# Optimization experiments

Measured on AMD Instinct MI355X. Metric: run time of the kernel, lower is better.

Reference implementation:

```python
import jax, jax.numpy as jnp
import numpy as np

TABLE_NUM = 16
TABLE_SIZE_LOG2 = 12
T = 1 << TABLE_SIZE_LOG2          # 4096 entries per table
FEAT = 2                          # features per entry (mini_linear in = table_num*2)
Z_DIM = 512
RES_MIN = 16
RES_MAX = 256
IMG = 256
MLP_HIDDEN = 64
OUT_DIM = 3
BATCH = 8
PRIME_Y = np.uint32(2654435761)   # instant-NGP spatial hash prime


def setup_inputs() -> dict:
    key = jax.random.key(0)
    ks = jax.random.split(key, 9)
    d_tab = TABLE_NUM * T * FEAT
    return {
        "z": jax.random.normal(ks[0], (BATCH, Z_DIM), jnp.float32),
        "w_table": jax.random.normal(ks[1], (Z_DIM, d_tab), jnp.float32) * 1e-2,
        "b_table": jnp.zeros((d_tab,), jnp.float32),
        "w1": jax.random.normal(ks[2], (TABLE_NUM * FEAT, MLP_HIDDEN), jnp.float32) * (1.0 / np.sqrt(TABLE_NUM * FEAT)),
        "b1": jnp.zeros((MLP_HIDDEN,), jnp.float32),
        "w2": jax.random.normal(ks[3], (MLP_HIDDEN, MLP_HIDDEN), jnp.float32) * (1.0 / np.sqrt(MLP_HIDDEN)),
        "b2": jnp.zeros((MLP_HIDDEN,), jnp.float32),
        "w3": jax.random.normal(ks[4], (MLP_HIDDEN, OUT_DIM), jnp.float32) * (1.0 / np.sqrt(MLP_HIDDEN)),
        "b3": jnp.zeros((OUT_DIM,), jnp.float32),
    }


def _sample_coords(b):
    c = (jnp.arange(IMG, dtype=jnp.float32) + 0.5) / IMG
    xx, yy = jnp.meshgrid(c, c, indexing="ij")  # torch.meshgrid default
    coords = jnp.stack([xx, yy], axis=-1).reshape(1, -1, 2)
    return jnp.broadcast_to(coords, (b, IMG * IMG, 2))


def _hash_retrieve(tables, coords):
    """tables: B x L x T x F; coords: B x N x 2 in [0,1). Returns B x N x (L*F)."""
    B, L, _, _ = tables.shape
    growth = np.exp((np.log(RES_MAX) - np.log(RES_MIN)) / (L - 1))
    offs = jnp.array([[0, 0], [1, 0], [0, 1], [1, 1]], dtype=jnp.uint32)  # 4 corners
    bidx = jnp.arange(B)[:, None, None]
    feats = []
    for l in range(L):
        res = jnp.float32(RES_MIN * (growth ** l))
        pos = coords * res                      # B,N,2
        pos0 = jnp.floor(pos)
        frac = pos - pos0                       # B,N,2
        corner = pos0.astype(jnp.uint32)[:, :, None, :] + offs[None, None]  # B,N,4,2
        idx = (corner[..., 0] ^ (corner[..., 1] * PRIME_Y)) & jnp.uint32(T - 1)
        f = tables[:, l][bidx, idx.astype(jnp.int32)]        # B,N,4,F gather
        fx, fy = frac[..., 0], frac[..., 1]
        w = jnp.stack([(1 - fx) * (1 - fy), fx * (1 - fy),
                       (1 - fx) * fy,       fx * fy], axis=-1)  # B,N,4
        feats.append(jnp.einsum("bncf,bnc->bnf", f, w))
    return jnp.concatenate(feats, axis=-1)


def reference(z, w_table, b_table, w1, b1, w2, b2, w3, b3):
    B = z.shape[0]
    tables = (z @ w_table + b_table).reshape(B, TABLE_NUM, T, FEAT)
    coords = _sample_coords(B).astype(tables.dtype)
    feat = _hash_retrieve(tables, coords)                    # B,N,L*F
    h = jax.nn.relu(feat @ w1 + b1)
    h = jax.nn.relu(h @ w2 + b2)
    o = jnp.tanh(h @ w3 + b3)                                # B,N,3
    return o.reshape(B, IMG, IMG, OUT_DIM).transpose(0, 3, 1, 2)
```

## Files before the change

### kernel.cpp

```cpp
#include <hip/hip_runtime.h>
#include <cmath>

#define TABLE_NUM 16
#define T_SIZE    4096
#define Z_DIM     512
#define IMG       256
#define D_TAB     (TABLE_NUM * T_SIZE * 2)
#define BATCH     8
#define HID       64
#define N_PIX     (IMG * IMG)
#define PRIME_Y   2654435761u
#define KCHUNK    4
#define KLEN      (Z_DIM / KCHUNK)
#define NG4       (D_TAB / 4)

typedef _Float16 v8h  __attribute__((ext_vector_type(8)));
typedef _Float16 v2h  __attribute__((ext_vector_type(2)));
typedef float    v4f  __attribute__((ext_vector_type(4)));

struct ResArr { float r[TABLE_NUM]; };

__global__ void prep_weights(const float* __restrict__ w1, const float* __restrict__ w2,
                             const float* __restrict__ w3, const float* __restrict__ z,
                             _Float16* __restrict__ w1T, _Float16* __restrict__ w2T,
                             _Float16* __restrict__ w3T, float* __restrict__ zT)
{
    const int t = threadIdx.x;
    for (int i = t; i < HID * 32; i += 256) {
        int n = i >> 5, k = i & 31;
        w1T[i] = (_Float16)w1[k * HID + n];
    }
    for (int i = t; i < HID * HID; i += 256) {
        int n = i >> 6, k = i & 63;
        w2T[i] = (_Float16)w2[k * HID + n];
    }
    for (int i = t; i < 16 * HID; i += 256) {
        int n = i >> 6, k = i & 63;
        w3T[i] = (_Float16)(n < 3 ? w3[k * 3 + n] : 0.f);
    }
    for (int i = t; i < Z_DIM * BATCH; i += 256) {
        int k = i >> 3, b = i & 7;
        zT[i] = z[b * Z_DIM + k];
    }
}

__global__ __launch_bounds__(256) void gen_partial(
    const float* __restrict__ zT, const float* __restrict__ w,
    float* __restrict__ part)
{
    const int c  = blockIdx.x >> 7;
    const int g  = (blockIdx.x & 127) * 256 + threadIdx.x;
    const int k0 = c * KLEN;
    const float4* wp = reinterpret_cast<const float4*>(w) + g;

    float4 acc[BATCH];
#pragma unroll
    for (int b = 0; b < BATCH; ++b) acc[b] = make_float4(0.f, 0.f, 0.f, 0.f);

#pragma unroll 8
    for (int kk = 0; kk < KLEN; ++kk) {
        const int k = k0 + kk;
        float4 wv = wp[(size_t)k * NG4];
        const float* zr = zT + k * BATCH;
#pragma unroll
        for (int b = 0; b < BATCH; ++b) {
            float zv = zr[b];
            acc[b].x = fmaf(zv, wv.x, acc[b].x);
            acc[b].y = fmaf(zv, wv.y, acc[b].y);
            acc[b].z = fmaf(zv, wv.z, acc[b].z);
            acc[b].w = fmaf(zv, wv.w, acc[b].w);
        }
    }

    float4* pp = reinterpret_cast<float4*>(part);
#pragma unroll
    for (int b = 0; b < BATCH; ++b)
        pp[((size_t)(c * BATCH + b) << 15) + g] = acc[b];
}

__global__ __launch_bounds__(256) void gen_reduce(
    const float* __restrict__ part, const float* __restrict__ bt,
    float* __restrict__ tabs)
{
    const int i = blockIdx.x * 256 + threadIdx.x;
    const int b = i >> 15, g = i & (NG4 - 1);
    const float4* pp = reinterpret_cast<const float4*>(part);

    float4 s = pp[((size_t)(0 * BATCH + b) << 15) + g];
#pragma unroll
    for (int c = 1; c < KCHUNK; ++c) {
        float4 p = pp[((size_t)(c * BATCH + b) << 15) + g];
        s.x += p.x; s.y += p.y; s.z += p.z; s.w += p.w;
    }
    float4 bv = reinterpret_cast<const float4*>(bt)[g];
    s.x += bv.x; s.y += bv.y; s.z += bv.z; s.w += bv.w;
    reinterpret_cast<float4*>(tabs)[((size_t)b << 15) + g] = s;
}

__global__ __launch_bounds__(256) void hash_mlp(
    const float* __restrict__ tabs,
    const _Float16* __restrict__ w1T, const _Float16* __restrict__ w2T,
    const _Float16* __restrict__ w3T,
    const float* __restrict__ b1, const float* __restrict__ b2,
    const float* __restrict__ b3,
    float* __restrict__ out, ResArr res)
{
    __shared__ _Float16 mbuf[4][64][72];
    const int tid  = threadIdx.x;
    const int wid  = tid >> 6;
    const int lane = tid & 63;
    const int b    = blockIdx.x & 7;
    const int tile = blockIdx.x >> 3;
    const int ti   = tile >> 4;
    const int tj   = tile & 15;
    const int i0   = ti * 16 + wid * 4;
    const int j0   = tj * 16;

    const int di = lane >> 4, dj = lane & 15;
    const float cx = ((float)(i0 + di) + 0.5f) * (1.0f / IMG);
    const float cy = ((float)(j0 + dj) + 0.5f) * (1.0f / IMG);
    const float* tb = tabs + (size_t)b * D_TAB;
    const float2* tb2 = reinterpret_cast<const float2*>(tb);

#pragma unroll 4
    for (int l = 0; l < TABLE_NUM; ++l) {
        float r  = res.r[l];
        float px = cx * r, py = cy * r;
        float fx0 = floorf(px), fy0 = floorf(py);
        float fx = px - fx0, fy = py - fy0;
        unsigned x0 = (unsigned)(int)fx0, y0 = (unsigned)(int)fy0;
        unsigned hy0 = y0 * PRIME_Y, hy1 = (y0 + 1u) * PRIME_Y;
        unsigned i00 = (x0 ^ hy0) & (T_SIZE - 1);
        unsigned i10 = ((x0 + 1u) ^ hy0) & (T_SIZE - 1);
        unsigned i01 = (x0 ^ hy1) & (T_SIZE - 1);
        unsigned i11 = ((x0 + 1u) ^ hy1) & (T_SIZE - 1);
        const float2* tl = tb2 + l * T_SIZE;
        float2 f00 = tl[i00], f10 = tl[i10], f01 = tl[i01], f11 = tl[i11];
        float w00 = (1.f - fx) * (1.f - fy);
        float w10 = fx * (1.f - fy);
        float w01 = (1.f - fx) * fy;
        float w11 = fx * fy;
        float e0 = f00.x * w00 + f10.x * w10 + f01.x * w01 + f11.x * w11;
        float e1 = f00.y * w00 + f10.y * w10 + f01.y * w01 + f11.y * w11;
        v2h p; p.x = (_Float16)e0; p.y = (_Float16)e1;
        *reinterpret_cast<v2h*>(&mbuf[wid][lane][2 * l]) = p;
    }

    const int arow = lane & 15;
    const int kgrp = lane >> 4;

    float bias1v[4], bias2v[4];
#pragma unroll
    for (int nt = 0; nt < 4; ++nt) {
        bias1v[nt] = b1[nt * 16 + arow];
        bias2v[nt] = b2[nt * 16 + arow];
    }
    const float bias3 = (arow < 3) ? b3[arow] : 0.f;

    v8h bf1[4], bf2a[4], bf2b[4];
#pragma unroll
    for (int nt = 0; nt < 4; ++nt) {
        bf1[nt]  = *reinterpret_cast<const v8h*>(&w1T[(nt * 16 + arow) * 32 + kgrp * 8]);
        bf2a[nt] = *reinterpret_cast<const v8h*>(&w2T[(nt * 16 + arow) * 64 + kgrp * 8]);
        bf2b[nt] = *reinterpret_cast<const v8h*>(&w2T[(nt * 16 + arow) * 64 + 32 + kgrp * 8]);
    }
    v8h bf3a = *reinterpret_cast<const v8h*>(&w3T[arow * 64 + kgrp * 8]);
    v8h bf3b = *reinterpret_cast<const v8h*>(&w3T[arow * 64 + 32 + kgrp * 8]);

    v8h a1[4];
#pragma unroll
    for (int mt = 0; mt < 4; ++mt)
        a1[mt] = *reinterpret_cast<const v8h*>(&mbuf[wid][mt * 16 + arow][kgrp * 8]);

    v4f c1[4][4];
#pragma unroll
    for (int nt = 0; nt < 4; ++nt)
#pragma unroll
        for (int mt = 0; mt < 4; ++mt) {
            v4f c = {0.f, 0.f, 0.f, 0.f};
            c = __builtin_amdgcn_mfma_f32_16x16x32_f16(a1[mt], bf1[nt], c, 0, 0, 0);
#pragma unroll
            for (int e = 0; e < 4; ++e)
                c1[mt][nt][e] = fmaxf(c[e] + bias1v[nt], 0.f);
        }

#pragma unroll
    for (int mt = 0; mt < 4; ++mt)
#pragma unroll
        for (int nt = 0; nt < 4; ++nt)
#pragma unroll
            for (int e = 0; e < 4; ++e)
                mbuf[wid][mt * 16 + kgrp * 4 + e][nt * 16 + arow] = (_Float16)c1[mt][nt][e];

    v8h a2[4][2];
#pragma unroll
    for (int mt = 0; mt < 4; ++mt) {
        a2[mt][0] = *reinterpret_cast<const v8h*>(&mbuf[wid][mt * 16 + arow][kgrp * 8]);
        a2[mt][1] = *reinterpret_cast<const v8h*>(&mbuf[wid][mt * 16 + arow][32 + kgrp * 8]);
    }
    v4f c2[4][4];
#pragma unroll
    for (int nt = 0; nt < 4; ++nt)
#pragma unroll
        for (int mt = 0; mt < 4; ++mt) {
            v4f c = {0.f, 0.f, 0.f, 0.f};
            c = __builtin_amdgcn_mfma_f32_16x16x32_f16(a2[mt][0], bf2a[nt], c, 0, 0, 0);
            c = __builtin_amdgcn_mfma_f32_16x16x32_f16(a2[mt][1], bf2b[nt], c, 0, 0, 0);
#pragma unroll
            for (int e = 0; e < 4; ++e)
                c2[mt][nt][e] = fmaxf(c[e] + bias2v[nt], 0.f);
        }

#pragma unroll
    for (int mt = 0; mt < 4; ++mt)
#pragma unroll
        for (int nt = 0; nt < 4; ++nt)
#pragma unroll
            for (int e = 0; e < 4; ++e)
                mbuf[wid][mt * 16 + kgrp * 4 + e][nt * 16 + arow] = (_Float16)c2[mt][nt][e];

#pragma unroll
    for (int mt = 0; mt < 4; ++mt) {
        v8h a0  = *reinterpret_cast<const v8h*>(&mbuf[wid][mt * 16 + arow][kgrp * 8]);
        v8h a1v = *reinterpret_cast<const v8h*>(&mbuf[wid][mt * 16 + arow][32 + kgrp * 8]);
        v4f c = {0.f, 0.f, 0.f, 0.f};
        c = __builtin_amdgcn_mfma_f32_16x16x32_f16(a0,  bf3a, c, 0, 0, 0);
        c = __builtin_amdgcn_mfma_f32_16x16x32_f16(a1v, bf3b, c, 0, 0, 0);
        if (arow < 3) {
            float4 st;
            st.x = tanhf(c[0] + bias3);
            st.y = tanhf(c[1] + bias3);
            st.z = tanhf(c[2] + bias3);
            st.w = tanhf(c[3] + bias3);
            size_t idx = ((size_t)b * 3 + arow) * N_PIX
                       + (size_t)(i0 + mt) * IMG + j0 + kgrp * 4;
            *reinterpret_cast<float4*>(&out[idx]) = st;
        }
    }
}

extern "C" void kernel_launch(void* const* d_in, const int* in_sizes, int n_in,
                              void* d_out, int out_size, void* d_ws, size_t ws_size,
                              hipStream_t stream)
{
    const float* z  = (const float*)d_in[0];
    const float* wt = (const float*)d_in[1];
    const float* bt = (const float*)d_in[2];
    const float* w1 = (const float*)d_in[3];
    const float* b1 = (const float*)d_in[4];
    const float* w2 = (const float*)d_in[5];
    const float* b2 = (const float*)d_in[6];
    const float* w3 = (const float*)d_in[7];
    const float* b3 = (const float*)d_in[8];
    float* out  = (float*)d_out;

    char* ws = (char*)d_ws;
    float*     tabs = (float*)ws;
    float*     part = (float*)(ws + (4 << 20));
    _Float16*  w1T  = (_Float16*)(ws + (20 << 20));
    _Float16*  w2T  = (_Float16*)(ws + (20 << 20) + 4096);
    _Float16*  w3T  = (_Float16*)(ws + (20 << 20) + 12288);
    float*     zT   = (float*)(ws + (20 << 20) + 16384);

    ResArr ra;
    const double growth = std::exp((std::log(256.0) - std::log(16.0)) / 15.0);
    for (int l = 0; l < TABLE_NUM; ++l)
        ra.r[l] = (float)(16.0 * std::pow(growth, (double)l));

    prep_weights<<<1, 256, 0, stream>>>(w1, w2, w3, z, w1T, w2T, w3T, zT);
    gen_partial<<<KCHUNK * (NG4 / 256), 256, 0, stream>>>(zT, wt, part);
    gen_reduce<<<BATCH * NG4 / 256, 256, 0, stream>>>(part, bt, tabs);
    hash_mlp<<<BATCH * (N_PIX / 256), 256, 0, stream>>>(
        tabs, w1T, w2T, w3T, b1, b2, b3, out, ra);
}
```

Before: 99.37 us.

## Stage per-tile hash-grid cells in LDS before bilinear interpolation

For each 16x16 pixel tile, the block first gathers every hash-table entry its pixels can touch at each of the 16 levels into a shared-memory buffer, sized by a per-level cell capacity. Each pixel then reads its four corners from LDS instead of issuing four scattered global gathers per level. This aims to cut redundant global and L2 gather traffic, since neighbouring pixels share corners. In exchange it adds about 10 KB of LDS per block, a block-wide barrier and a staging phase, and it relies on the hard-coded capacities covering every tile footprint.

```diff
diff --git a/kernel.cpp b/kernel.cpp
--- a/kernel.cpp
+++ b/kernel.cpp
@@ -20,6 +20,10 @@
 
 struct ResArr { float r[TABLE_NUM]; };
 
+__device__ constexpr int WCAP[16]  = {3,4,4,4,5,5,5,6,7,8,9,10,11,13,15,18};
+__device__ constexpr int CBASE[16] = {0,9,25,41,57,82,107,132,168,217,281,362,462,583,752,977};
+#define CTOT 1301
+
 __global__ void prep_weights(const float* __restrict__ w1, const float* __restrict__ w2,
                              const float* __restrict__ w3, const float* __restrict__ z,
                              _Float16* __restrict__ w1T, _Float16* __restrict__ w2T,
@@ -86,7 +90,7 @@
     const int b = i >> 15, g = i & (NG4 - 1);
     const float4* pp = reinterpret_cast<const float4*>(part);
 
-    float4 s = pp[((size_t)(0 * BATCH + b) << 15) + g];
+    float4 s = pp[((size_t)b << 15) + g];
 #pragma unroll
     for (int c = 1; c < KCHUNK; ++c) {
         float4 p = pp[((size_t)(c * BATCH + b) << 15) + g];
@@ -106,36 +110,56 @@
     float* __restrict__ out, ResArr res)
 {
     __shared__ _Float16 mbuf[4][64][72];
+    __shared__ float2   cstage[CTOT];
+
     const int tid  = threadIdx.x;
     const int wid  = tid >> 6;
     const int lane = tid & 63;
     const int b    = blockIdx.x & 7;
     const int tile = blockIdx.x >> 3;
-    const int ti   = tile >> 4;
-    const int tj   = tile & 15;
-    const int i0   = ti * 16 + wid * 4;
-    const int j0   = tj * 16;
+    const int i0b  = (tile >> 4) * 16;
+    const int j0b  = (tile & 15) * 16;
+    const int i0   = i0b + wid * 4;
 
     const int di = lane >> 4, dj = lane & 15;
-    const float cx = ((float)(i0 + di) + 0.5f) * (1.0f / IMG);
-    const float cy = ((float)(j0 + dj) + 0.5f) * (1.0f / IMG);
-    const float* tb = tabs + (size_t)b * D_TAB;
-    const float2* tb2 = reinterpret_cast<const float2*>(tb);
-
-#pragma unroll 4
+    const float cxp = ((float)(i0 + di) + 0.5f) * (1.0f / IMG);
+    const float cyp = ((float)(j0b + dj) + 0.5f) * (1.0f / IMG);
+    const float2* tb2 = reinterpret_cast<const float2*>(tabs + (size_t)b * D_TAB);
+
+    const float cx_lo = ((float)i0b + 0.5f) * (1.0f / IMG);
+    const float cy_lo = ((float)j0b + 0.5f) * (1.0f / IMG);
+
+#pragma unroll
     for (int l = 0; l < TABLE_NUM; ++l) {
-        float r  = res.r[l];
-        float px = cx * r, py = cy * r;
+        const float r  = res.r[l];
+        const int   xs = (int)floorf(cx_lo * r);
+        const int   ys = (int)floorf(cy_lo * r);
+        const float2* tl = tb2 + l * T_SIZE;
+        const int W = WCAP[l], CNT = WCAP[l] * WCAP[l];
+        for (int e = tid; e < CNT; e += 256) {
+            int yy = e / W, xx = e - yy * W;
+            unsigned idx = ((unsigned)(xs + xx) ^
+                            ((unsigned)(ys + yy) * PRIME_Y)) & (T_SIZE - 1);
+            cstage[CBASE[l] + e] = tl[idx];
+        }
+    }
+    __syncthreads();
+
+#pragma unroll
+    for (int l = 0; l < TABLE_NUM; ++l) {
+        const float r   = res.r[l];
+        const float xsf = floorf(cx_lo * r);
+        const float ysf = floorf(cy_lo * r);
+        float px = cxp * r, py = cyp * r;
         float fx0 = floorf(px), fy0 = floorf(py);
         float fx = px - fx0, fy = py - fy0;
-        unsigned x0 = (unsigned)(int)fx0, y0 = (unsigned)(int)fy0;
-        unsigned hy0 = y0 * PRIME_Y, hy1 = (y0 + 1u) * PRIME_Y;
-        unsigned i00 = (x0 ^ hy0) & (T_SIZE - 1);
-        unsigned i10 = ((x0 + 1u) ^ hy0) & (T_SIZE - 1);
-        unsigned i01 = (x0 ^ hy1) & (T_SIZE - 1);
-        unsigned i11 = ((x0 + 1u) ^ hy1) & (T_SIZE - 1);
-        const float2* tl = tb2 + l * T_SIZE;
-        float2 f00 = tl[i00], f10 = tl[i10], f01 = tl[i01], f11 = tl[i11];
+        int xi = (int)(fx0 - xsf), yi = (int)(fy0 - ysf);
+        const float2* cb = cstage + CBASE[l];
+        const int W = WCAP[l];
+        float2 f00 = cb[yi * W + xi];
+        float2 f10 = cb[yi * W + xi + 1];
+        float2 f01 = cb[(yi + 1) * W + xi];
+        float2 f11 = cb[(yi + 1) * W + xi + 1];
         float w00 = (1.f - fx) * (1.f - fy);
         float w10 = fx * (1.f - fy);
         float w01 = (1.f - fx) * fy;
@@ -233,7 +257,7 @@
             st.z = tanhf(c[2] + bias3);
             st.w = tanhf(c[3] + bias3);
             size_t idx = ((size_t)b * 3 + arow) * N_PIX
-                       + (size_t)(i0 + mt) * IMG + j0 + kgrp * 4;
+                       + (size_t)(i0 + mt) * IMG + j0b + kgrp * 4;
             *reinterpret_cast<float4*>(&out[idx]) = st;
         }
     }
```

Result: no change. 99.41 us (+0.0%).
